# Kernel tuning notes

Measured on AMD Instinct MI355X. Metric: run time of the kernel, lower is better.

The kernel has to match this reference:

```python
import jax, jax.numpy as jnp
import numpy as np

B, J, E = 4096, 32, 256

def setup_inputs() -> dict:
    key = jax.random.key(0)
    ks = jax.random.split(key, 7)
    return {
        "x": jax.random.normal(ks[0], (B, E), dtype=jnp.float32),
        "state": jax.random.normal(ks[1], (B, J * E), dtype=jnp.float32),
        "keys": jax.random.normal(ks[2], (J, E), dtype=jnp.float32) * 0.1,
        "U": jax.random.normal(ks[3], (E, E), dtype=jnp.float32) * 0.1,
        "V": jax.random.normal(ks[4], (E, E), dtype=jnp.float32) * 0.1,
        "W": jax.random.normal(ks[5], (E, E), dtype=jnp.float32) * 0.1,
        "bias": jax.random.normal(ks[6], (E,), dtype=jnp.float32) * 0.1,
    }

def reference(x, state, keys, U, V, W, bias):
    b, je = state.shape
    j = keys.shape[0]
    e = x.shape[1]
    s = state.reshape(b, j, e)                      # [B,J,E]
    # gate_j = sigmoid(<x, state_j> + <x, key_j>)
    gate = jax.nn.sigmoid(jnp.einsum('be,bje->bj', x, s)
                          + x @ keys.T)             # [B,J]
    # candidate_j = relu(U s_j + bias + W x + V k_j)
    cand = jax.nn.relu(jnp.einsum('bje,fe->bjf', s, U)
                       + bias
                       + (x @ W.T)[:, None, :]
                       + (keys @ V.T)[None, :, :])  # [B,J,E]
    s_next = s + gate[..., None] * cand
    norm = jnp.abs(jnp.linalg.norm(s_next, axis=-1, keepdims=True)) + 1e-8
    s_next = s_next / norm
    return s_next.reshape(b, je)
```

## Files before the change

### kernel.cpp

```cpp
#include <hip/hip_runtime.h>
#include <hip/hip_bf16.h>

typedef __bf16 bf16_t;
typedef __attribute__((ext_vector_type(8))) __bf16 bf16x8;
typedef __attribute__((ext_vector_type(4))) float f32x4;

#define E_DIM 256
#define J_DIM 32
#define B_DIM 4096
#define M_DIM (B_DIM * J_DIM)
#define BM 64
#define BK 32
#define LDA 40
#define LDB 40
#define LDAF 33

__device__ inline bf16x8 cvt8(const float* __restrict__ p) {
    f32x4 a = *(const f32x4*)p;
    f32x4 b = *(const f32x4*)(p + 4);
    bf16x8 r;
    r[0] = (bf16_t)a[0]; r[1] = (bf16_t)a[1]; r[2] = (bf16_t)a[2]; r[3] = (bf16_t)a[3];
    r[4] = (bf16_t)b[0]; r[5] = (bf16_t)b[1]; r[6] = (bf16_t)b[2]; r[7] = (bf16_t)b[3];
    return r;
}

__global__ __launch_bounds__(256) void vkb_kernel(const float* __restrict__ keys,
                                                  const float* __restrict__ V,
                                                  const float* __restrict__ bias,
                                                  float* __restrict__ vkb) {
    int j = blockIdx.x, f = threadIdx.x;
    __shared__ float sk[E_DIM];
    sk[f] = keys[j * E_DIM + f];
    __syncthreads();
    float acc = bias[f];
    for (int e = 0; e < E_DIM; e += 4) {
        f32x4 vv = *(const f32x4*)(V + (size_t)f * E_DIM + e);
#pragma unroll
        for (int i = 0; i < 4; ++i) acc += vv[i] * sk[e + i];
    }
    vkb[(size_t)j * E_DIM + f] = acc;
}

__global__ __launch_bounds__(256) void xk_kernel(const float* __restrict__ x,
                                                 const float* __restrict__ keys,
                                                 float* __restrict__ xk) {
    __shared__ __align__(16) float sK[J_DIM][E_DIM];
    __shared__ __align__(16) float sX[8][E_DIM];
    int tid = threadIdx.x;
    int b0 = blockIdx.x * 8;
#pragma unroll
    for (int it = 0; it < 8; ++it) {
        int t = it * 256 + tid;
        *(f32x4*)(&sK[0][0] + (size_t)t * 4) = *(const f32x4*)(keys + (size_t)t * 4);
    }
#pragma unroll
    for (int it = 0; it < 2; ++it) {
        int t = it * 256 + tid;
        *(f32x4*)(&sX[0][0] + (size_t)t * 4) =
            *(const f32x4*)(x + (size_t)b0 * E_DIM + (size_t)t * 4);
    }
    __syncthreads();
    int j = tid & 31, bl = tid >> 5;
    float acc = 0.f;
    for (int e = 0; e < E_DIM; e += 4) {
        f32x4 xv = *(const f32x4*)(&sX[bl][e]);
        f32x4 kv = *(const f32x4*)(&sK[j][e]);
#pragma unroll
        for (int i = 0; i < 4; ++i) acc += xv[i] * kv[i];
    }
    xk[(size_t)(b0 + bl) * J_DIM + j] = acc;
}

__global__ __launch_bounds__(256) void wx_kernel(const float* __restrict__ x,
                                                 const float* __restrict__ W,
                                                 float* __restrict__ wx) {
    __shared__ __align__(16) bf16_t sA[BM][LDA];
    __shared__ __align__(16) bf16_t sB[E_DIM][LDB];
    int tid = threadIdx.x;
    int w = tid >> 6, lane = tid & 63, quad = lane >> 4, l15 = lane & 15;
    int m0 = blockIdx.x * BM;
    f32x4 acc[16];
#pragma unroll
    for (int nt = 0; nt < 16; ++nt)
#pragma unroll
        for (int r = 0; r < 4; ++r) acc[nt][r] = 0.f;
    int arow = tid >> 2, akk = (tid & 3) * 8;
    for (int kc = 0; kc < 8; ++kc) {
        int k0 = kc * BK;
        __syncthreads();
        *(bf16x8*)(&sA[arow][akk]) = cvt8(x + (size_t)(m0 + arow) * E_DIM + k0 + akk);
#pragma unroll
        for (int it = 0; it < 4; ++it) {
            int t = it * 256 + tid;
            int n = t >> 2, kk = (t & 3) * 8;
            *(bf16x8*)(&sB[n][kk]) = cvt8(W + (size_t)n * E_DIM + k0 + kk);
        }
        __syncthreads();
        bf16x8 af = *(const bf16x8*)(&sA[w * 16 + l15][quad * 8]);
#pragma unroll
        for (int nt = 0; nt < 16; ++nt) {
            bf16x8 bfr = *(const bf16x8*)(&sB[nt * 16 + l15][quad * 8]);
            acc[nt] = __builtin_amdgcn_mfma_f32_16x16x32_bf16(af, bfr, acc[nt], 0, 0, 0);
        }
    }
#pragma unroll
    for (int nt = 0; nt < 16; ++nt)
#pragma unroll
        for (int r = 0; r < 4; ++r)
            wx[(size_t)(m0 + w * 16 + quad * 4 + r) * E_DIM + nt * 16 + l15] = acc[nt][r];
}

__global__ __launch_bounds__(256) void memcell_kernel(
    const float* __restrict__ x, const float* __restrict__ state,
    const float* __restrict__ U, const float* __restrict__ wx,
    const float* __restrict__ xk, const float* __restrict__ vkb,
    float* __restrict__ out) {
    __shared__ __align__(16) bf16_t sA[BM][LDA];
    __shared__ __align__(16) bf16_t sB[E_DIM][LDB];
    __shared__ __align__(16) bf16_t sX[2][E_DIM];
    __shared__ __align__(16) float sAf[BM][LDAF];
    __shared__ __align__(16) float sXf[2][E_DIM];
    int tid = threadIdx.x;
    int w = tid >> 6, lane = tid & 63, quad = lane >> 4, l15 = lane & 15;
    int m0 = blockIdx.x * BM;
    int b0 = m0 >> 5;
    f32x4 acc[16];
#pragma unroll
    for (int nt = 0; nt < 16; ++nt)
#pragma unroll
        for (int r = 0; r < 4; ++r) acc[nt][r] = 0.f;
    float gdot = 0.f;
    if (tid < 64) {
        int bb = tid >> 5, p = tid & 31;
        f32x4 xa = *(const f32x4*)(x + (size_t)(b0 + bb) * E_DIM + p * 8);
        f32x4 xb = *(const f32x4*)(x + (size_t)(b0 + bb) * E_DIM + p * 8 + 4);
        *(f32x4*)(&sXf[bb][p * 8]) = xa;
        *(f32x4*)(&sXf[bb][p * 8 + 4]) = xb;
        bf16x8 r;
        r[0] = (bf16_t)xa[0]; r[1] = (bf16_t)xa[1]; r[2] = (bf16_t)xa[2]; r[3] = (bf16_t)xa[3];
        r[4] = (bf16_t)xb[0]; r[5] = (bf16_t)xb[1]; r[6] = (bf16_t)xb[2]; r[7] = (bf16_t)xb[3];
        *(bf16x8*)(&sX[bb][p * 8]) = r;
    }
    int arow = tid >> 2, akk = (tid & 3) * 8;
    for (int kc = 0; kc < 8; ++kc) {
        int k0 = kc * BK;
        __syncthreads();
        {
            const float* sp = state + (size_t)(m0 + arow) * E_DIM + k0 + akk;
            f32x4 a = *(const f32x4*)sp;
            f32x4 b = *(const f32x4*)(sp + 4);
            *(f32x4*)(&sAf[arow][akk]) = a;
            *(f32x4*)(&sAf[arow][akk + 4]) = b;
            bf16x8 r;
            r[0] = (bf16_t)a[0]; r[1] = (bf16_t)a[1]; r[2] = (bf16_t)a[2]; r[3] = (bf16_t)a[3];
            r[4] = (bf16_t)b[0]; r[5] = (bf16_t)b[1]; r[6] = (bf16_t)b[2]; r[7] = (bf16_t)b[3];
            *(bf16x8*)(&sA[arow][akk]) = r;
        }
#pragma unroll
        for (int it = 0; it < 4; ++it) {
            int t = it * 256 + tid;
            int n = t >> 2, kk = (t & 3) * 8;
            *(bf16x8*)(&sB[n][kk]) = cvt8(U + (size_t)n * E_DIM + k0 + kk);
        }
        __syncthreads();
        bf16x8 af = *(const bf16x8*)(&sA[w * 16 + l15][quad * 8]);
#pragma unroll
        for (int i = 0; i < 8; ++i)
            gdot += sAf[w * 16 + l15][quad * 8 + i] * sXf[w >> 1][k0 + quad * 8 + i];
#pragma unroll
        for (int nt = 0; nt < 16; ++nt) {
            bf16x8 bfr = *(const bf16x8*)(&sB[nt * 16 + l15][quad * 8]);
            acc[nt] = __builtin_amdgcn_mfma_f32_16x16x32_bf16(af, bfr, acc[nt], 0, 0, 0);
        }
    }
    gdot += __shfl_xor(gdot, 16);
    gdot += __shfl_xor(gdot, 32);
    int bw = b0 + (w >> 1);
    float garg = gdot + xk[(size_t)bw * J_DIM + (w & 1) * 16 + l15];
    float gv = 1.f / (1.f + expf(-garg));
    float gate[4];
#pragma unroll
    for (int r = 0; r < 4; ++r) gate[r] = __shfl(gv, quad * 4 + r);
    float sumsq[4] = {0.f, 0.f, 0.f, 0.f};
    const float* wxrow = wx + (size_t)bw * E_DIM;
#pragma unroll
    for (int nt = 0; nt < 16; ++nt) {
        int f = nt * 16 + l15;
        float wxf = wxrow[f];
#pragma unroll
        for (int r = 0; r < 4; ++r) {
            int rl = quad * 4 + r;
            int jidx = (w & 1) * 16 + rl;
            float c = acc[nt][r] + wxf + vkb[(size_t)jidx * E_DIM + f];
            c = fmaxf(c, 0.f);
            float sv = state[(size_t)(m0 + w * 16 + rl) * E_DIM + f];
            float t = fmaf(gate[r], c, sv);
            acc[nt][r] = t;
            sumsq[r] += t * t;
        }
    }
    float rn[4];
#pragma unroll
    for (int r = 0; r < 4; ++r) {
        float s2 = sumsq[r];
        s2 += __shfl_xor(s2, 1);
        s2 += __shfl_xor(s2, 2);
        s2 += __shfl_xor(s2, 4);
        s2 += __shfl_xor(s2, 8);
        rn[r] = 1.f / (sqrtf(s2) + 1e-8f);
    }
#pragma unroll
    for (int nt = 0; nt < 16; ++nt)
#pragma unroll
        for (int r = 0; r < 4; ++r)
            out[(size_t)(m0 + w * 16 + quad * 4 + r) * E_DIM + nt * 16 + l15] =
                acc[nt][r] * rn[r];
}

extern "C" void kernel_launch(void* const* d_in, const int* in_sizes, int n_in,
                              void* d_out, int out_size, void* d_ws, size_t ws_size,
                              hipStream_t stream) {
    const float* x     = (const float*)d_in[0];
    const float* state = (const float*)d_in[1];
    const float* keys  = (const float*)d_in[2];
    const float* U     = (const float*)d_in[3];
    const float* V     = (const float*)d_in[4];
    const float* W     = (const float*)d_in[5];
    const float* bias  = (const float*)d_in[6];
    float* out = (float*)d_out;

    float* wsf = (float*)d_ws;
    float* wx  = wsf;
    float* xk  = wsf + (size_t)B_DIM * E_DIM;
    float* vkb = xk + (size_t)B_DIM * J_DIM;

    vkb_kernel<<<J_DIM, 256, 0, stream>>>(keys, V, bias, vkb);
    xk_kernel<<<B_DIM / 8, 256, 0, stream>>>(x, keys, xk);
    wx_kernel<<<B_DIM / BM, 256, 0, stream>>>(x, W, wx);
    memcell_kernel<<<M_DIM / BM, 256, 0, stream>>>(x, state, U, wx, xk, vkb, out);
}
```

Measured before the change: 340.6 us.

## Drop LDS staging; pre-convert U/W to bf16 and fuse prep kernels

Merges the vkb, xk and new U/W bf16-conversion work into one prep kernel launch. The GEMM kernels no longer stage tiles in shared memory. They load MFMA fragments directly from global memory: state is prefetched one k-step ahead in registers, and the pre-converted bf16 U/W are read from cache. This removes the LDS round trips, the __syncthreads barriers and the per-block repeated conversion of U. The cost is more global/L2 traffic for the B operand, since every block rereads U through uncoalesced 16-byte strided loads.

Result: slower. 464.0 us (+36.2%).

```diff
diff --git a/kernel.cpp b/kernel.cpp
--- a/kernel.cpp
+++ b/kernel.cpp
@@ -3,103 +3,107 @@
 
 typedef __bf16 bf16_t;
 typedef __attribute__((ext_vector_type(8))) __bf16 bf16x8;
+typedef __attribute__((ext_vector_type(4))) __bf16 bf16x4;
 typedef __attribute__((ext_vector_type(4))) float f32x4;
 
 #define E_DIM 256
 #define J_DIM 32
 #define B_DIM 4096
 #define M_DIM (B_DIM * J_DIM)
-#define BM 64
-#define BK 32
-#define LDA 40
-#define LDB 40
-#define LDAF 33
-
-__device__ inline bf16x8 cvt8(const float* __restrict__ p) {
-    f32x4 a = *(const f32x4*)p;
-    f32x4 b = *(const f32x4*)(p + 4);
-    bf16x8 r;
-    r[0] = (bf16_t)a[0]; r[1] = (bf16_t)a[1]; r[2] = (bf16_t)a[2]; r[3] = (bf16_t)a[3];
-    r[4] = (bf16_t)b[0]; r[5] = (bf16_t)b[1]; r[6] = (bf16_t)b[2]; r[7] = (bf16_t)b[3];
-    return r;
-}
-
-__global__ __launch_bounds__(256) void vkb_kernel(const float* __restrict__ keys,
-                                                  const float* __restrict__ V,
-                                                  const float* __restrict__ bias,
-                                                  float* __restrict__ vkb) {
-    int j = blockIdx.x, f = threadIdx.x;
-    __shared__ float sk[E_DIM];
-    sk[f] = keys[j * E_DIM + f];
-    __syncthreads();
-    float acc = bias[f];
-    for (int e = 0; e < E_DIM; e += 4) {
-        f32x4 vv = *(const f32x4*)(V + (size_t)f * E_DIM + e);
-#pragma unroll
-        for (int i = 0; i < 4; ++i) acc += vv[i] * sk[e + i];
-    }
-    vkb[(size_t)j * E_DIM + f] = acc;
-}
-
-__global__ __launch_bounds__(256) void xk_kernel(const float* __restrict__ x,
-                                                 const float* __restrict__ keys,
-                                                 float* __restrict__ xk) {
-    __shared__ __align__(16) float sK[J_DIM][E_DIM];
-    __shared__ __align__(16) float sX[8][E_DIM];
+
+#define XK_BLOCKS 512
+#define CVT_BLOCKS 64
+#define VKB_BLOCKS 32
+#define PREP_GRID (XK_BLOCKS + 2 * CVT_BLOCKS + VKB_BLOCKS)
+
+#define XK_LDA (E_DIM + 4)
+
+__global__ __launch_bounds__(256) void prep_kernel(
+    const float* __restrict__ x, const float* __restrict__ keys,
+    const float* __restrict__ U, const float* __restrict__ V,
+    const float* __restrict__ W, const float* __restrict__ bias,
+    float* __restrict__ xk, float* __restrict__ vkb,
+    bf16_t* __restrict__ Ubf, bf16_t* __restrict__ Wbf) {
+    __shared__ float smem[(J_DIM + 8) * XK_LDA];
     int tid = threadIdx.x;
-    int b0 = blockIdx.x * 8;
-#pragma unroll
-    for (int it = 0; it < 8; ++it) {
-        int t = it * 256 + tid;
-        *(f32x4*)(&sK[0][0] + (size_t)t * 4) = *(const f32x4*)(keys + (size_t)t * 4);
-    }
-#pragma unroll
-    for (int it = 0; it < 2; ++it) {
-        int t = it * 256 + tid;
-        *(f32x4*)(&sX[0][0] + (size_t)t * 4) =
-            *(const f32x4*)(x + (size_t)b0 * E_DIM + (size_t)t * 4);
-    }
-    __syncthreads();
-    int j = tid & 31, bl = tid >> 5;
-    float acc = 0.f;
-    for (int e = 0; e < E_DIM; e += 4) {
-        f32x4 xv = *(const f32x4*)(&sX[bl][e]);
-        f32x4 kv = *(const f32x4*)(&sK[j][e]);
-#pragma unroll
-        for (int i = 0; i < 4; ++i) acc += xv[i] * kv[i];
-    }
-    xk[(size_t)(b0 + bl) * J_DIM + j] = acc;
+    int bid = blockIdx.x;
+    if (bid < XK_BLOCKS) {
+        float* sK = smem;
+        float* sX = smem + J_DIM * XK_LDA;
+        int b0 = bid * 8;
+#pragma unroll
+        for (int it = 0; it < 8; ++it) {
+            int t = it * 256 + tid;
+            int r = t >> 6, c = (t & 63) * 4;
+            *(f32x4*)(sK + r * XK_LDA + c) = *(const f32x4*)(keys + (size_t)r * E_DIM + c);
+        }
+#pragma unroll
+        for (int it = 0; it < 2; ++it) {
+            int t = it * 256 + tid;
+            int r = t >> 6, c = (t & 63) * 4;
+            *(f32x4*)(sX + r * XK_LDA + c) =
+                *(const f32x4*)(x + (size_t)(b0 + r) * E_DIM + c);
+        }
+        __syncthreads();
+        int j = tid & 31, bl = tid >> 5;
+        float acc = 0.f;
+        for (int e = 0; e < E_DIM; e += 4) {
+            f32x4 xv = *(const f32x4*)(sX + bl * XK_LDA + e);
+            f32x4 kv = *(const f32x4*)(sK + j * XK_LDA + e);
+#pragma unroll
+            for (int i = 0; i < 4; ++i) acc += xv[i] * kv[i];
+        }
+        xk[(size_t)(b0 + bl) * J_DIM + j] = acc;
+    } else if (bid < XK_BLOCKS + 2 * CVT_BLOCKS) {
+        int cb = bid - XK_BLOCKS;
+        const float* src = (cb < CVT_BLOCKS) ? U : W;
+        bf16_t* dst = (cb < CVT_BLOCKS) ? Ubf : Wbf;
+        int idx = (cb & (CVT_BLOCKS - 1)) * 1024 + tid * 4;
+        f32x4 v = *(const f32x4*)(src + idx);
+        bf16x4 o;
+#pragma unroll
+        for (int i = 0; i < 4; ++i) o[i] = (bf16_t)v[i];
+        *(bf16x4*)(dst + idx) = o;
+    } else {
+        int j = bid - (XK_BLOCKS + 2 * CVT_BLOCKS);
+        int f = tid;
+        float* sk = smem;
+        sk[f] = keys[(size_t)j * E_DIM + f];
+        __syncthreads();
+        float acc = bias[f];
+        for (int e = 0; e < E_DIM; e += 4) {
+            f32x4 vv = *(const f32x4*)(V + (size_t)f * E_DIM + e);
+#pragma unroll
+            for (int i = 0; i < 4; ++i) acc += vv[i] * sk[e + i];
+        }
+        vkb[(size_t)j * E_DIM + f] = acc;
+    }
 }
 
 __global__ __launch_bounds__(256) void wx_kernel(const float* __restrict__ x,
-                                                 const float* __restrict__ W,
+                                                 const bf16_t* __restrict__ Wbf,
                                                  float* __restrict__ wx) {
-    __shared__ __align__(16) bf16_t sA[BM][LDA];
-    __shared__ __align__(16) bf16_t sB[E_DIM][LDB];
     int tid = threadIdx.x;
     int w = tid >> 6, lane = tid & 63, quad = lane >> 4, l15 = lane & 15;
-    int m0 = blockIdx.x * BM;
+    int m0 = blockIdx.x * 64;
     f32x4 acc[16];
 #pragma unroll
     for (int nt = 0; nt < 16; ++nt)
 #pragma unroll
         for (int r = 0; r < 4; ++r) acc[nt][r] = 0.f;
-    int arow = tid >> 2, akk = (tid & 3) * 8;
+    const float* ap = x + (size_t)(m0 + w * 16 + l15) * E_DIM + quad * 8;
+    const bf16_t* bp = Wbf + (size_t)l15 * E_DIM + quad * 8;
+#pragma unroll
     for (int kc = 0; kc < 8; ++kc) {
-        int k0 = kc * BK;
-        __syncthreads();
-        *(bf16x8*)(&sA[arow][akk]) = cvt8(x + (size_t)(m0 + arow) * E_DIM + k0 + akk);
-#pragma unroll
-        for (int it = 0; it < 4; ++it) {
-            int t = it * 256 + tid;
-            int n = t >> 2, kk = (t & 3) * 8;
-            *(bf16x8*)(&sB[n][kk]) = cvt8(W + (size_t)n * E_DIM + k0 + kk);
-        }
-        __syncthreads();
-        bf16x8 af = *(const bf16x8*)(&sA[w * 16 + l15][quad * 8]);
+        int k0 = kc * 32;
+        f32x4 a0 = *(const f32x4*)(ap + k0);
+        f32x4 a1 = *(const f32x4*)(ap + k0 + 4);
+        bf16x8 af;
+#pragma unroll
+        for (int i = 0; i < 4; ++i) { af[i] = (bf16_t)a0[i]; af[4 + i] = (bf16_t)a1[i]; }
 #pragma unroll
         for (int nt = 0; nt < 16; ++nt) {
-            bf16x8 bfr = *(const bf16x8*)(&sB[nt * 16 + l15][quad * 8]);
+            bf16x8 bfr = *(const bf16x8*)(bp + k0 + nt * 16 * E_DIM);
             acc[nt] = __builtin_amdgcn_mfma_f32_16x16x32_bf16(af, bfr, acc[nt], 0, 0, 0);
         }
     }
@@ -112,70 +116,48 @@
 
 __global__ __launch_bounds__(256) void memcell_kernel(
     const float* __restrict__ x, const float* __restrict__ state,
-    const float* __restrict__ U, const float* __restrict__ wx,
+    const bf16_t* __restrict__ Ubf, const float* __restrict__ wx,
     const float* __restrict__ xk, const float* __restrict__ vkb,
     float* __restrict__ out) {
-    __shared__ __align__(16) bf16_t sA[BM][LDA];
-    __shared__ __align__(16) bf16_t sB[E_DIM][LDB];
-    __shared__ __align__(16) bf16_t sX[2][E_DIM];
-    __shared__ __align__(16) float sAf[BM][LDAF];
-    __shared__ __align__(16) float sXf[2][E_DIM];
     int tid = threadIdx.x;
     int w = tid >> 6, lane = tid & 63, quad = lane >> 4, l15 = lane & 15;
-    int m0 = blockIdx.x * BM;
-    int b0 = m0 >> 5;
+    int m0 = blockIdx.x * 64;
+    int bw = (m0 >> 5) + (w >> 1);
     f32x4 acc[16];
 #pragma unroll
     for (int nt = 0; nt < 16; ++nt)
 #pragma unroll
         for (int r = 0; r < 4; ++r) acc[nt][r] = 0.f;
     float gdot = 0.f;
-    if (tid < 64) {
-        int bb = tid >> 5, p = tid & 31;
-        f32x4 xa = *(const f32x4*)(x + (size_t)(b0 + bb) * E_DIM + p * 8);
-        f32x4 xb = *(const f32x4*)(x + (size_t)(b0 + bb) * E_DIM + p * 8 + 4);
-        *(f32x4*)(&sXf[bb][p * 8]) = xa;
-        *(f32x4*)(&sXf[bb][p * 8 + 4]) = xb;
-        bf16x8 r;
-        r[0] = (bf16_t)xa[0]; r[1] = (bf16_t)xa[1]; r[2] = (bf16_t)xa[2]; r[3] = (bf16_t)xa[3];
-        r[4] = (bf16_t)xb[0]; r[5] = (bf16_t)xb[1]; r[6] = (bf16_t)xb[2]; r[7] = (bf16_t)xb[3];
-        *(bf16x8*)(&sX[bb][p * 8]) = r;
-    }
-    int arow = tid >> 2, akk = (tid & 3) * 8;
+    const float* sp = state + (size_t)(m0 + w * 16 + l15) * E_DIM + quad * 8;
+    const float* xp = x + (size_t)bw * E_DIM + quad * 8;
+    const bf16_t* up = Ubf + (size_t)l15 * E_DIM + quad * 8;
+    f32x4 a0 = *(const f32x4*)sp;
+    f32x4 a1 = *(const f32x4*)(sp + 4);
+#pragma unroll
     for (int kc = 0; kc < 8; ++kc) {
-        int k0 = kc * BK;
-        __syncthreads();
-        {
-            const float* sp = state + (size_t)(m0 + arow) * E_DIM + k0 + akk;
-            f32x4 a = *(const f32x4*)sp;
-            f32x4 b = *(const f32x4*)(sp + 4);
-            *(f32x4*)(&sAf[arow][akk]) = a;
-            *(f32x4*)(&sAf[arow][akk + 4]) = b;
-            bf16x8 r;
-            r[0] = (bf16_t)a[0]; r[1] = (bf16_t)a[1]; r[2] = (bf16_t)a[2]; r[3] = (bf16_t)a[3];
-            r[4] = (bf16_t)b[0]; r[5] = (bf16_t)b[1]; r[6] = (bf16_t)b[2]; r[7] = (bf16_t)b[3];
-            *(bf16x8*)(&sA[arow][akk]) = r;
-        }
-#pragma unroll
-        for (int it = 0; it < 4; ++it) {
-            int t = it * 256 + tid;
-            int n = t >> 2, kk = (t & 3) * 8;
-            *(bf16x8*)(&sB[n][kk]) = cvt8(U + (size_t)n * E_DIM + k0 + kk);
-        }
-        __syncthreads();
-        bf16x8 af = *(const bf16x8*)(&sA[w * 16 + l15][quad * 8]);
-#pragma unroll
-        for (int i = 0; i < 8; ++i)
-            gdot += sAf[w * 16 + l15][quad * 8 + i] * sXf[w >> 1][k0 + quad * 8 + i];
+        int k0 = kc * 32;
+        int kn = ((kc + 1) & 7) * 32;
+        f32x4 n0 = *(const f32x4*)(sp + kn);
+        f32x4 n1 = *(const f32x4*)(sp + kn + 4);
+        f32x4 xv0 = *(const f32x4*)(xp + k0);
+        f32x4 xv1 = *(const f32x4*)(xp + k0 + 4);
+        bf16x8 af;
+#pragma unroll
+        for (int i = 0; i < 4; ++i) { af[i] = (bf16_t)a0[i]; af[4 + i] = (bf16_t)a1[i]; }
+#pragma unroll
+        for (int i = 0; i < 4; ++i) gdot += a0[i] * xv0[i];
+#pragma unroll
+        for (int i = 0; i < 4; ++i) gdot += a1[i] * xv1[i];
 #pragma unroll
         for (int nt = 0; nt < 16; ++nt) {
-            bf16x8 bfr = *(const bf16x8*)(&sB[nt * 16 + l15][quad * 8]);
+            bf16x8 bfr = *(const bf16x8*)(up + k0 + nt * 16 * E_DIM);
             acc[nt] = __builtin_amdgcn_mfma_f32_16x16x32_bf16(af, bfr, acc[nt], 0, 0, 0);
         }
+        a0 = n0; a1 = n1;
     }
     gdot += __shfl_xor(gdot, 16);
     gdot += __shfl_xor(gdot, 32);
-    int bw = b0 + (w >> 1);
     float garg = gdot + xk[(size_t)bw * J_DIM + (w & 1) * 16 + l15];
     float gv = 1.f / (1.f + expf(-garg));
     float gate[4];
@@ -233,9 +215,10 @@
     float* wx  = wsf;
     float* xk  = wsf + (size_t)B_DIM * E_DIM;
     float* vkb = xk + (size_t)B_DIM * J_DIM;
-
-    vkb_kernel<<<J_DIM, 256, 0, stream>>>(keys, V, bias, vkb);
-    xk_kernel<<<B_DIM / 8, 256, 0, stream>>>(x, keys, xk);
-    wx_kernel<<<B_DIM / BM, 256, 0, stream>>>(x, W, wx);
-    memcell_kernel<<<M_DIM / BM, 256, 0, stream>>>(x, state, U, wx, xk, vkb, out);
-}
+    bf16_t* Ubf = (bf16_t*)(vkb + (size_t)J_DIM * E_DIM);
+    bf16_t* Wbf = Ubf + (size_t)E_DIM * E_DIM;
+
+    prep_kernel<<<PREP_GRID, 256, 0, stream>>>(x, keys, U, V, W, bias, xk, vkb, Ubf, Wbf);
+    wx_kernel<<<B_DIM / 64, 256, 0, stream>>>(x, Wbf, wx);
+    memcell_kernel<<<M_DIM / 64, 256, 0, stream>>>(x, state, Ubf, wx, xk, vkb, out);
+}
```

## Merge xk/vkb prologue kernels, split wx GEMM over N, pad shared rows

Applied to the files above, without the earlier changes.

The xk and vkb precompute kernels are merged into one launch whose blocks branch on blockIdx, removing a kernel launch. The xk shared-memory rows get padding to cut bank conflicts. The wx GEMM is split four ways along N, so 256 blocks run instead of 64, with less shared memory and fewer accumulators per block. An unused bf16 copy of x is dropped from the main kernel. The prologue kernels are small next to the main memcell GEMM over the full state tensor, so the overall effect is probably limited.

Measured after the change: 309.4 us. -9.2%, faster.

```diff
diff --git a/kernel.cpp b/kernel.cpp
--- a/kernel.cpp
+++ b/kernel.cpp
@@ -15,6 +15,8 @@
 #define LDB 40
 #define LDAF 33
 
+#define XK_LDA (E_DIM + 4)
+
 __device__ inline bf16x8 cvt8(const float* __restrict__ p) {
     f32x4 a = *(const f32x4*)p;
     f32x4 b = *(const f32x4*)(p + 4);
@@ -24,64 +26,65 @@
     return r;
 }
 
-__global__ __launch_bounds__(256) void vkb_kernel(const float* __restrict__ keys,
-                                                  const float* __restrict__ V,
-                                                  const float* __restrict__ bias,
-                                                  float* __restrict__ vkb) {
-    int j = blockIdx.x, f = threadIdx.x;
-    __shared__ float sk[E_DIM];
-    sk[f] = keys[j * E_DIM + f];
-    __syncthreads();
-    float acc = bias[f];
-    for (int e = 0; e < E_DIM; e += 4) {
-        f32x4 vv = *(const f32x4*)(V + (size_t)f * E_DIM + e);
-#pragma unroll
-        for (int i = 0; i < 4; ++i) acc += vv[i] * sk[e + i];
-    }
-    vkb[(size_t)j * E_DIM + f] = acc;
-}
-
-__global__ __launch_bounds__(256) void xk_kernel(const float* __restrict__ x,
-                                                 const float* __restrict__ keys,
-                                                 float* __restrict__ xk) {
-    __shared__ __align__(16) float sK[J_DIM][E_DIM];
-    __shared__ __align__(16) float sX[8][E_DIM];
-    int tid = threadIdx.x;
-    int b0 = blockIdx.x * 8;
-#pragma unroll
-    for (int it = 0; it < 8; ++it) {
-        int t = it * 256 + tid;
-        *(f32x4*)(&sK[0][0] + (size_t)t * 4) = *(const f32x4*)(keys + (size_t)t * 4);
-    }
-#pragma unroll
-    for (int it = 0; it < 2; ++it) {
-        int t = it * 256 + tid;
-        *(f32x4*)(&sX[0][0] + (size_t)t * 4) =
-            *(const f32x4*)(x + (size_t)b0 * E_DIM + (size_t)t * 4);
-    }
-    __syncthreads();
-    int j = tid & 31, bl = tid >> 5;
-    float acc = 0.f;
-    for (int e = 0; e < E_DIM; e += 4) {
-        f32x4 xv = *(const f32x4*)(&sX[bl][e]);
-        f32x4 kv = *(const f32x4*)(&sK[j][e]);
-#pragma unroll
-        for (int i = 0; i < 4; ++i) acc += xv[i] * kv[i];
-    }
-    xk[(size_t)(b0 + bl) * J_DIM + j] = acc;
+__global__ __launch_bounds__(256) void xkvkb_kernel(
+    const float* __restrict__ x, const float* __restrict__ keys,
+    const float* __restrict__ V, const float* __restrict__ bias,
+    float* __restrict__ xk, float* __restrict__ vkb) {
+    __shared__ float smem[(J_DIM + 8) * XK_LDA];
+    int tid = threadIdx.x, bid = blockIdx.x;
+    if (bid < 512) {
+        float* sK = smem;
+        float* sX = smem + J_DIM * XK_LDA;
+        int b0 = bid * 8;
+#pragma unroll
+        for (int it = 0; it < 8; ++it) {
+            int t = it * 256 + tid;
+            int r = t >> 6, c = (t & 63) * 4;
+            *(f32x4*)(sK + r * XK_LDA + c) = *(const f32x4*)(keys + (size_t)r * E_DIM + c);
+        }
+#pragma unroll
+        for (int it = 0; it < 2; ++it) {
+            int t = it * 256 + tid;
+            int r = t >> 6, c = (t & 63) * 4;
+            *(f32x4*)(sX + r * XK_LDA + c) =
+                *(const f32x4*)(x + (size_t)b0 * E_DIM + (size_t)r * E_DIM + c);
+        }
+        __syncthreads();
+        int j = tid & 31, bl = tid >> 5;
+        float acc = 0.f;
+        for (int e = 0; e < E_DIM; e += 4) {
+            f32x4 xv = *(const f32x4*)(sX + bl * XK_LDA + e);
+            f32x4 kv = *(const f32x4*)(sK + j * XK_LDA + e);
+#pragma unroll
+            for (int i = 0; i < 4; ++i) acc += xv[i] * kv[i];
+        }
+        xk[(size_t)(b0 + bl) * J_DIM + j] = acc;
+    } else {
+        int j = bid - 512, f = tid;
+        float* sk = smem;
+        sk[f] = keys[(size_t)j * E_DIM + f];
+        __syncthreads();
+        float acc = bias[f];
+        for (int e = 0; e < E_DIM; e += 4) {
+            f32x4 vv = *(const f32x4*)(V + (size_t)f * E_DIM + e);
+#pragma unroll
+            for (int i = 0; i < 4; ++i) acc += vv[i] * sk[e + i];
+        }
+        vkb[(size_t)j * E_DIM + f] = acc;
+    }
 }
 
 __global__ __launch_bounds__(256) void wx_kernel(const float* __restrict__ x,
                                                  const float* __restrict__ W,
                                                  float* __restrict__ wx) {
     __shared__ __align__(16) bf16_t sA[BM][LDA];
-    __shared__ __align__(16) bf16_t sB[E_DIM][LDB];
+    __shared__ __align__(16) bf16_t sBw[64][LDB];
     int tid = threadIdx.x;
     int w = tid >> 6, lane = tid & 63, quad = lane >> 4, l15 = lane & 15;
-    int m0 = blockIdx.x * BM;
-    f32x4 acc[16];
-#pragma unroll
-    for (int nt = 0; nt < 16; ++nt)
+    int m0 = (blockIdx.x >> 2) * BM, n0 = (blockIdx.x & 3) * 64;
+    f32x4 acc[4];
+#pragma unroll
+    for (int nt = 0; nt < 4; ++nt)
 #pragma unroll
         for (int r = 0; r < 4; ++r) acc[nt][r] = 0.f;
     int arow = tid >> 2, akk = (tid & 3) * 8;
@@ -89,25 +92,21 @@
         int k0 = kc * BK;
         __syncthreads();
         *(bf16x8*)(&sA[arow][akk]) = cvt8(x + (size_t)(m0 + arow) * E_DIM + k0 + akk);
-#pragma unroll
-        for (int it = 0; it < 4; ++it) {
-            int t = it * 256 + tid;
-            int n = t >> 2, kk = (t & 3) * 8;
-            *(bf16x8*)(&sB[n][kk]) = cvt8(W + (size_t)n * E_DIM + k0 + kk);
-        }
+        *(bf16x8*)(&sBw[arow][akk]) = cvt8(W + (size_t)(n0 + arow) * E_DIM + k0 + akk);
         __syncthreads();
         bf16x8 af = *(const bf16x8*)(&sA[w * 16 + l15][quad * 8]);
 #pragma unroll
-        for (int nt = 0; nt < 16; ++nt) {
-            bf16x8 bfr = *(const bf16x8*)(&sB[nt * 16 + l15][quad * 8]);
+        for (int nt = 0; nt < 4; ++nt) {
+            bf16x8 bfr = *(const bf16x8*)(&sBw[nt * 16 + l15][quad * 8]);
             acc[nt] = __builtin_amdgcn_mfma_f32_16x16x32_bf16(af, bfr, acc[nt], 0, 0, 0);
         }
     }
 #pragma unroll
-    for (int nt = 0; nt < 16; ++nt)
+    for (int nt = 0; nt < 4; ++nt)
 #pragma unroll
         for (int r = 0; r < 4; ++r)
-            wx[(size_t)(m0 + w * 16 + quad * 4 + r) * E_DIM + nt * 16 + l15] = acc[nt][r];
+            wx[(size_t)(m0 + w * 16 + quad * 4 + r) * E_DIM + n0 + nt * 16 + l15] =
+                acc[nt][r];
 }
 
 __global__ __launch_bounds__(256) void memcell_kernel(
@@ -117,7 +116,6 @@
     float* __restrict__ out) {
     __shared__ __align__(16) bf16_t sA[BM][LDA];
     __shared__ __align__(16) bf16_t sB[E_DIM][LDB];
-    __shared__ __align__(16) bf16_t sX[2][E_DIM];
     __shared__ __align__(16) float sAf[BM][LDAF];
     __shared__ __align__(16) float sXf[2][E_DIM];
     int tid = threadIdx.x;
@@ -136,10 +134,6 @@
         f32x4 xb = *(const f32x4*)(x + (size_t)(b0 + bb) * E_DIM + p * 8 + 4);
         *(f32x4*)(&sXf[bb][p * 8]) = xa;
         *(f32x4*)(&sXf[bb][p * 8 + 4]) = xb;
-        bf16x8 r;
-        r[0] = (bf16_t)xa[0]; r[1] = (bf16_t)xa[1]; r[2] = (bf16_t)xa[2]; r[3] = (bf16_t)xa[3];
-        r[4] = (bf16_t)xb[0]; r[5] = (bf16_t)xb[1]; r[6] = (bf16_t)xb[2]; r[7] = (bf16_t)xb[3];
-        *(bf16x8*)(&sX[bb][p * 8]) = r;
     }
     int arow = tid >> 2, akk = (tid & 3) * 8;
     for (int kc = 0; kc < 8; ++kc) {
@@ -234,8 +228,7 @@
     float* xk  = wsf + (size_t)B_DIM * E_DIM;
     float* vkb = xk + (size_t)B_DIM * J_DIM;
 
-    vkb_kernel<<<J_DIM, 256, 0, stream>>>(keys, V, bias, vkb);
-    xk_kernel<<<B_DIM / 8, 256, 0, stream>>>(x, keys, xk);
-    wx_kernel<<<B_DIM / BM, 256, 0, stream>>>(x, W, wx);
+    xkvkb_kernel<<<544, 256, 0, stream>>>(x, keys, V, bias, xk, vkb);
+    wx_kernel<<<256, 256, 0, stream>>>(x, W, wx);
     memcell_kernel<<<M_DIM / BM, 256, 0, stream>>>(x, state, U, wx, xk, vkb, out);
 }
```
